# Performance work log

Hardware: AMD Instinct MI355X
Metric: run time of the kernel (lower is better)

Reference implementation:

```python
import jax, jax.numpy as jnp
import numpy as np

N_NODES = 100000
N_EDGES = 1250000
D_IN = 64
D_OUT = 64


def setup_inputs() -> dict:
    key = jax.random.key(0)
    k1, k2, k3, k4, k5 = jax.random.split(key, 5)
    x = jax.random.normal(k1, (N_NODES, D_IN), dtype=jnp.float32)
    edge_index = jax.random.randint(k2, (2, N_EDGES), 0, N_NODES, dtype=jnp.int64)
    # Linear weights stored torch-style as [out, in]
    w_neigh = jax.random.normal(k3, (D_OUT, D_IN), dtype=jnp.float32) / np.sqrt(D_IN)
    w_self = jax.random.normal(k4, (D_OUT, D_IN), dtype=jnp.float32) / np.sqrt(D_IN)
    b_self = jax.random.normal(k5, (D_OUT,), dtype=jnp.float32) * 0.01
    return {"x": x, "edge_index": edge_index, "w_neigh": w_neigh, "w_self": w_self, "b_self": b_self}


def reference(x, edge_index, w_neigh, w_self, b_self):
    num_nodes = x.shape[0]
    src, dst = edge_index[0], edge_index[1]
    # mean aggregation of neighbor features: scatter-add then divide by in-degree
    agg = jax.ops.segment_sum(x[src], dst, num_segments=num_nodes)  # [N, d]
    degree = jax.ops.segment_sum(jnp.ones_like(dst, dtype=x.dtype), dst, num_segments=num_nodes)
    degree = jnp.maximum(degree, 1.0)
    agg = agg / degree[:, None]
    return agg @ w_neigh.T + x @ w_self.T + b_self
```

## Files before the change

kernel.cpp:

```cpp
#include <hip/hip_runtime.h>

#define N_NODES 100000
#define N_EDGES 1250000
#define D 64
#define BSH 6
#define BNODES 64
#define NB 1563
#define WSW 68
#define G 512
#define CHUNK 2444
#define MM_BLOCKS ((N_NODES + 127) / 128)
#define BIN_BLOCKS 128
#define BIN_CHUNK ((N_EDGES + BIN_BLOCKS - 1) / BIN_BLOCKS)

typedef unsigned int u32;
typedef short bf16x8 __attribute__((ext_vector_type(8)));
typedef float f32x4 __attribute__((ext_vector_type(4)));

__device__ __forceinline__ u32 pack_bf16(float lo, float hi) {
    u32 a = __float_as_uint(lo);
    u32 b = __float_as_uint(hi);
    a = (a + 0x7fffu + ((a >> 16) & 1u)) >> 16;
    b = (b + 0x7fffu + ((b >> 16) & 1u)) >> 16;
    return a | (b << 16);
}

__global__ void __launch_bounds__(256) k_histw(const int* __restrict__ ei,
                                               u32* __restrict__ ghist,
                                               const float* __restrict__ wn,
                                               const float* __restrict__ wsf,
                                               u32* __restrict__ bfrag) {
    __shared__ u32 hist[NB];
    int tid = threadIdx.x;
    if (blockIdx.x < G) {
        int g = blockIdx.x;
        int e0 = g * CHUNK, e1 = min(e0 + CHUNK, N_EDGES);
        for (int i = tid; i < NB; i += 256) hist[i] = 0;
        __syncthreads();
        const int4* dp = (const int4*)(ei + N_EDGES + e0);
        int nv = (e1 - e0) >> 2;
        for (int i = tid; i < nv; i += 256) {
            int4 d4 = dp[i];
            atomicAdd(&hist[d4.x >> BSH], 1u);
            atomicAdd(&hist[d4.y >> BSH], 1u);
            atomicAdd(&hist[d4.z >> BSH], 1u);
            atomicAdd(&hist[d4.w >> BSH], 1u);
        }
        __syncthreads();
        for (int i = tid; i < NB; i += 256)
            ghist[(size_t)i * G + g] = hist[i];
    } else {
        for (int i = tid; i < 4096; i += 256) {
            int t = i >> 9, h = (i >> 8) & 1, l = (i >> 2) & 63, q = i & 3;
            int k0 = h * 32 + (l >> 4) * 8 + 2 * q;
            int n = t * 16 + (l & 15);
            const float* w = (n < 64) ? &wn[(size_t)n * 64] : &wsf[(size_t)(n - 64) * 64];
            bfrag[i] = pack_bf16(w[k0], w[k0 + 1]);
        }
    }
}

__global__ void __launch_bounds__(512) k_scanB(const u32* __restrict__ ghist,
                                               u32* __restrict__ gbase,
                                               u32* __restrict__ bcnt) {
    __shared__ u32 wt[8];
    int t = threadIdx.x;
    int b = blockIdx.x;
    int lane = t & 63, wv = t >> 6;
    u32 v = ghist[(size_t)b * G + t];
    u32 s = v;
#pragma unroll
    for (int off = 1; off < 64; off <<= 1) {
        u32 n = __shfl_up(s, off, 64);
        if (lane >= off) s += n;
    }
    if (lane == 63) wt[wv] = s;
    __syncthreads();
    u32 add = 0;
#pragma unroll
    for (int q = 0; q < 8; ++q) add += (q < wv) ? wt[q] : 0u;
    u32 incl = s + add;
    gbase[(size_t)b * G + t] = incl - v;
    if (t == G - 1) bcnt[b] = incl;
}

__global__ void __launch_bounds__(256) k_scatmm(const int* __restrict__ ei,
                                                const u32* __restrict__ gbase,
                                                u32* __restrict__ binned,
                                                int cap,
                                                const float* __restrict__ x,
                                                const u32* __restrict__ bfrag,
                                                const float* __restrict__ bias,
                                                u32* __restrict__ y16,
                                                float* __restrict__ zout) {
    __shared__ u32 cur[NB];
    int tid = threadIdx.x;
    if (blockIdx.x < G) {
        int g = blockIdx.x;
        int e0 = g * CHUNK, e1 = min(e0 + CHUNK, N_EDGES);
        for (int i = tid; i < NB; i += 256)
            cur[i] = gbase[(size_t)i * G + g];
        __syncthreads();
        const int4* sp = (const int4*)(ei + e0);
        const int4* dp = (const int4*)(ei + N_EDGES + e0);
        int nv = (e1 - e0) >> 2;
        for (int i = tid; i < nv; i += 256) {
            int4 s4 = sp[i];
            int4 d4 = dp[i];
            int ss[4] = {s4.x, s4.y, s4.z, s4.w};
            int dd[4] = {d4.x, d4.y, d4.z, d4.w};
#pragma unroll
            for (int u = 0; u < 4; ++u) {
                int b = dd[u] >> BSH;
                u32 loc = atomicAdd(&cur[b], 1u);
                if (loc < (u32)cap)
                    binned[(size_t)b * cap + loc] = ((u32)ss[u] << BSH) | (u32)(dd[u] & (BNODES - 1));
            }
        }
        return;
    }

    int w = tid >> 6, l = tid & 63;
    int lg = l >> 4, c = l & 15;
    int nodebase = (blockIdx.x - G) * 128 + w * 32;

    union FU { uint4 u; bf16x8 v; };

    bf16x8 af[2][2];
#pragma unroll
    for (int m = 0; m < 2; ++m) {
        int node = nodebase + m * 16 + c;
        if (node >= N_NODES) node = N_NODES - 1;
        const float4* xr = (const float4*)(x + (size_t)node * D);
#pragma unroll
        for (int h = 0; h < 2; ++h) {
            float4 p0 = xr[h * 8 + lg * 2];
            float4 p1 = xr[h * 8 + lg * 2 + 1];
            FU au;
            au.u.x = pack_bf16(p0.x, p0.y);
            au.u.y = pack_bf16(p0.z, p0.w);
            au.u.z = pack_bf16(p1.x, p1.y);
            au.u.w = pack_bf16(p1.z, p1.w);
            af[m][h] = au.v;
        }
    }

    f32x4 acc[2][8];
#pragma unroll
    for (int m = 0; m < 2; ++m) {
#pragma unroll
        for (int t = 0; t < 4; ++t) acc[m][t] = (f32x4){0.f, 0.f, 0.f, 0.f};
#pragma unroll
        for (int t = 4; t < 8; ++t) {
            float bb = bias[(t - 4) * 16 + c];
            acc[m][t] = (f32x4){bb, bb, bb, bb};
        }
    }

    const uint4* bp = (const uint4*)bfrag;
#pragma unroll
    for (int tc = 0; tc < 2; ++tc) {
        bf16x8 bf[4][2];
#pragma unroll
        for (int tt = 0; tt < 4; ++tt)
#pragma unroll
            for (int h = 0; h < 2; ++h) {
                FU bu;
                bu.u = bp[(((tc * 4 + tt) * 2 + h) * 64) + l];
                bf[tt][h] = bu.v;
            }
#pragma unroll
        for (int m = 0; m < 2; ++m)
#pragma unroll
            for (int tt = 0; tt < 4; ++tt) {
                int t = tc * 4 + tt;
                acc[m][t] = __builtin_amdgcn_mfma_f32_16x16x32_bf16(
                    af[m][0], bf[tt][0], acc[m][t], 0, 0, 0);
                acc[m][t] = __builtin_amdgcn_mfma_f32_16x16x32_bf16(
                    af[m][1], bf[tt][1], acc[m][t], 0, 0, 0);
            }
    }

#pragma unroll
    for (int m = 0; m < 2; ++m) {
        int rowbase = nodebase + m * 16 + lg * 4;
#pragma unroll
        for (int r = 0; r < 4; ++r) {
            int node = rowbase + r;
            bool ok = node < N_NODES;
#pragma unroll
            for (int t = 4; t < 8; ++t) {
                if (ok) zout[(size_t)node * D + (t - 4) * 16 + c] = acc[m][t][r];
            }
#pragma unroll
            for (int t = 0; t < 4; ++t) {
                float v = acc[m][t][r];
                float o = __shfl_xor(v, 1);
                if (ok && !(c & 1))
                    y16[(size_t)node * 32 + t * 8 + (c >> 1)] = pack_bf16(v, o);
            }
        }
    }
}

__global__ void __launch_bounds__(256) k_sortgather(const u32* __restrict__ y16,
                                                    const u32* __restrict__ binned,
                                                    const u32* __restrict__ bcnt,
                                                    int cap,
                                                    float* __restrict__ io) {
    __shared__ u32 eh[1024];
    __shared__ u32 srt[1024];
    __shared__ u32 hist[BNODES];
    __shared__ u32 nbase[BNODES];
    __shared__ u32 cur[BNODES];
    int tid = threadIdx.x;
    int b = blockIdx.x;
    int cnt = min((int)bcnt[b], cap);
    const u32* seg = binned + (size_t)b * cap;

    if (tid < BNODES) hist[tid] = 0;
    __syncthreads();
    const uint4* segv = (const uint4*)seg;
    int nv = cnt >> 2;
    for (int i = tid; i < nv; i += 256) {
        uint4 w4 = segv[i];
        *(uint4*)&eh[4 * i] = w4;
        atomicAdd(&hist[w4.x & (BNODES - 1)], 1u);
        atomicAdd(&hist[w4.y & (BNODES - 1)], 1u);
        atomicAdd(&hist[w4.z & (BNODES - 1)], 1u);
        atomicAdd(&hist[w4.w & (BNODES - 1)], 1u);
    }
    for (int i = (cnt & ~3) + tid; i < cnt; i += 256) {
        u32 w = seg[i];
        eh[i] = w;
        atomicAdd(&hist[w & (BNODES - 1)], 1u);
    }
    __syncthreads();
    if (tid < BNODES) {
        u32 v = hist[tid];
        u32 s = v;
#pragma unroll
        for (int off = 1; off < 64; off <<= 1) {
            u32 n = __shfl_up(s, off, 64);
            if (tid >= off) s += n;
        }
        u32 excl = s - v;
        nbase[tid] = excl;
        cur[tid] = excl;
    }
    __syncthreads();
    for (int i = tid; i < cnt; i += 256) {
        u32 w = eh[i];
        u32 p = atomicAdd(&cur[w & (BNODES - 1)], 1u);
        srt[p] = w >> BSH;
    }
    __syncthreads();

    int wv = tid >> 6, lane = tid & 63;
    int sub = lane >> 4;
    int pr = lane & 15;
    const uint2* yv = (const uint2*)y16;
    int nodebase = b << BSH;

    for (int i = 0; i < 16; ++i) {
        int dl = wv * 16 + i;
        int node = nodebase + dl;
        u32 o0 = nbase[dl];
        u32 dg = hist[dl];
        float a0 = 0.f, a1 = 0.f, a2 = 0.f, a3 = 0.f;
        for (u32 r = 0; r < dg; r += 32) {
            uint2 w[8];
#pragma unroll
            for (int t = 0; t < 8; ++t) {
                u32 e = r + 4 * t + sub;
                w[t] = make_uint2(0u, 0u);
                if (e < dg) w[t] = yv[(size_t)srt[o0 + e] * 16 + pr];
            }
#pragma unroll
            for (int t = 0; t < 8; ++t) {
                if (r + 4u * (u32)t < dg) {
                    a0 += __uint_as_float(w[t].x << 16);
                    a1 += __uint_as_float(w[t].x & 0xffff0000u);
                    a2 += __uint_as_float(w[t].y << 16);
                    a3 += __uint_as_float(w[t].y & 0xffff0000u);
                }
            }
        }
        a0 += __shfl_xor(a0, 16); a1 += __shfl_xor(a1, 16);
        a2 += __shfl_xor(a2, 16); a3 += __shfl_xor(a3, 16);
        a0 += __shfl_xor(a0, 32); a1 += __shfl_xor(a1, 32);
        a2 += __shfl_xor(a2, 32); a3 += __shfl_xor(a3, 32);
        if (sub == 0 && node < N_NODES) {
            float inv = 1.0f / (float)max(dg, 1u);
            float4 z = *(const float4*)&io[(size_t)node * D + 4 * pr];
            *(float4*)&io[(size_t)node * D + 4 * pr] =
                make_float4(z.x + a0 * inv, z.y + a1 * inv, z.z + a2 * inv, z.w + a3 * inv);
        }
    }
}

__global__ void __launch_bounds__(256) k_bin2(const int* __restrict__ ei,
                                              u32* __restrict__ bcnt,
                                              u32* __restrict__ binned,
                                              int cap) {
    __shared__ u32 hist[NB];
    __shared__ u32 rbase[NB];
    int tid = threadIdx.x;
    int e0 = blockIdx.x * BIN_CHUNK;
    int e1 = min(e0 + BIN_CHUNK, N_EDGES);
    const int* dstp = ei + N_EDGES;
    for (int i = tid; i < NB; i += 256) hist[i] = 0;
    __syncthreads();
    for (int e = e0 + tid; e < e1; e += 256)
        atomicAdd(&hist[dstp[e] >> BSH], 1u);
    __syncthreads();
    for (int i = tid; i < NB; i += 256) {
        u32 h = hist[i];
        rbase[i] = h ? atomicAdd(&bcnt[i], h) : 0u;
        hist[i] = 0;
    }
    __syncthreads();
    for (int e = e0 + tid; e < e1; e += 256) {
        int d = dstp[e];
        int s = ei[e];
        int b = d >> BSH;
        u32 loc = atomicAdd(&hist[b], 1u);
        u32 slot = rbase[b] + loc;
        if (slot < (u32)cap)
            binned[(size_t)b * cap + slot] = ((u32)s << BSH) | (u32)(d & (BNODES - 1));
    }
}

__global__ void __launch_bounds__(256) k_sort_fb(u32* __restrict__ binned,
                                                 const u32* __restrict__ bcnt,
                                                 int cap,
                                                 u32* __restrict__ offs,
                                                 u32* __restrict__ deg) {
    __shared__ u32 eh[1024];
    __shared__ u32 hist[BNODES];
    __shared__ u32 cur[BNODES];
    int tid = threadIdx.x;
    int b = blockIdx.x;
    int cnt = min((int)bcnt[b], cap);
    u32* seg = binned + (size_t)b * cap;
    if (tid < BNODES) hist[tid] = 0;
    __syncthreads();
    for (int i = tid; i < cnt; i += 256) {
        u32 w = seg[i];
        eh[i] = w;
        atomicAdd(&hist[w & (BNODES - 1)], 1u);
    }
    __syncthreads();
    if (tid < BNODES) {
        u32 v = hist[tid];
        u32 s = v;
#pragma unroll
        for (int off = 1; off < 64; off <<= 1) {
            u32 n = __shfl_up(s, off, 64);
            if (tid >= off) s += n;
        }
        u32 excl = s - v;
        cur[tid] = excl;
        int node = (b << BSH) + tid;
        if (node < N_NODES) {
            offs[node] = (u32)((size_t)b * cap + excl);
            deg[node] = v;
        }
    }
    __syncthreads();
    for (int i = tid; i < cnt; i += 256) {
        u32 w = eh[i];
        u32 p = atomicAdd(&cur[w & (BNODES - 1)], 1u);
        seg[p] = w >> BSH;
    }
}

__global__ void __launch_bounds__(256) k_gather32(const float* __restrict__ x,
                                                  const u32* __restrict__ binned,
                                                  const u32* __restrict__ offs,
                                                  const u32* __restrict__ deg,
                                                  float* __restrict__ agg) {
    int tid = blockIdx.x * 256 + threadIdx.x;
    int node = tid >> 6;
    int d = tid & 63;
    if (node >= N_NODES) return;
    u32 o0 = offs[node], dg = deg[node];
    u32 o1 = o0 + dg;
    float s = 0.f;
    u32 j = o0;
    for (; j + 8 <= o1; j += 8) {
        u32 e[8];
        float v[8];
#pragma unroll
        for (int t = 0; t < 8; ++t) e[t] = binned[j + t];
#pragma unroll
        for (int t = 0; t < 8; ++t) v[t] = x[(size_t)e[t] * D + d];
#pragma unroll
        for (int t = 0; t < 8; ++t) s += v[t];
    }
    for (; j < o1; ++j) s += x[(size_t)binned[j] * D + d];
    agg[(size_t)node * D + d] = s / (float)max(dg, 1u);
}

__global__ void __launch_bounds__(256) k_gemm_fb(const float* __restrict__ x,
                                                 const float* __restrict__ wn,
                                                 const float* __restrict__ wsf,
                                                 const float* __restrict__ bias,
                                                 float* __restrict__ io) {
    __shared__ float At[BNODES * WSW];
    __shared__ float Wt[128 * WSW];
    int tid = threadIdx.x;
    int base = blockIdx.x * 64;
    const float4* iop = (const float4*)io;
    const float4* xp  = (const float4*)x;
    for (int i = tid; i < 4096; i += 256) {
        int d = i >> 6, k = i & 63;
        Wt[k * WSW + d] = wn[i];
        Wt[(64 + k) * WSW + d] = wsf[i];
    }
    for (int i = tid; i < 1024; i += 256) {
        int r = i >> 4, q = i & 15;
        int node = base + r;
        float4 v = make_float4(0.f, 0.f, 0.f, 0.f);
        if (node < N_NODES) v = iop[(size_t)node * 16 + q];
        *(float4*)&At[r * WSW + q * 4] = v;
    }
    __syncthreads();
    int tn = tid >> 4, td = tid & 15;
    int n0 = tn * 4, d0 = td * 4;
    float4 b4 = *(const float4*)&bias[d0];
    float acc[4][4];
#pragma unroll
    for (int i = 0; i < 4; ++i) {
        acc[i][0] = b4.x; acc[i][1] = b4.y; acc[i][2] = b4.z; acc[i][3] = b4.w;
    }
#pragma unroll 8
    for (int kc = 0; kc < 16; ++kc) {
        float4 a[4], w[4];
#pragma unroll
        for (int i = 0; i < 4; ++i) a[i] = *(const float4*)&At[(n0 + i) * WSW + kc * 4];
#pragma unroll
        for (int t = 0; t < 4; ++t) w[t] = *(const float4*)&Wt[(kc * 4 + t) * WSW + d0];
#pragma unroll
        for (int i = 0; i < 4; ++i) {
            const float av[4] = {a[i].x, a[i].y, a[i].z, a[i].w};
#pragma unroll
            for (int t = 0; t < 4; ++t) {
                acc[i][0] += av[t] * w[t].x; acc[i][1] += av[t] * w[t].y;
                acc[i][2] += av[t] * w[t].z; acc[i][3] += av[t] * w[t].w;
            }
        }
    }
    __syncthreads();
    for (int i = tid; i < 1024; i += 256) {
        int r = i >> 4, q = i & 15;
        int node = base + r;
        float4 v = make_float4(0.f, 0.f, 0.f, 0.f);
        if (node < N_NODES) v = xp[(size_t)node * 16 + q];
        *(float4*)&At[r * WSW + q * 4] = v;
    }
    __syncthreads();
#pragma unroll 8
    for (int kc = 0; kc < 16; ++kc) {
        float4 a[4], w[4];
#pragma unroll
        for (int i = 0; i < 4; ++i) a[i] = *(const float4*)&At[(n0 + i) * WSW + kc * 4];
#pragma unroll
        for (int t = 0; t < 4; ++t) w[t] = *(const float4*)&Wt[(64 + kc * 4 + t) * WSW + d0];
#pragma unroll
        for (int i = 0; i < 4; ++i) {
            const float av[4] = {a[i].x, a[i].y, a[i].z, a[i].w};
#pragma unroll
            for (int t = 0; t < 4; ++t) {
                acc[i][0] += av[t] * w[t].x; acc[i][1] += av[t] * w[t].y;
                acc[i][2] += av[t] * w[t].z; acc[i][3] += av[t] * w[t].w;
            }
        }
    }
#pragma unroll
    for (int i = 0; i < 4; ++i) {
        int node = base + n0 + i;
        if (node < N_NODES) {
            *(float4*)&io[(size_t)node * D + d0] =
                make_float4(acc[i][0], acc[i][1], acc[i][2], acc[i][3]);
        }
    }
}

extern "C" void kernel_launch(void* const* d_in, const int* in_sizes, int n_in,
                              void* d_out, int out_size, void* d_ws, size_t ws_size,
                              hipStream_t stream) {
    const float* x = (const float*)d_in[0];
    const int* ei = (const int*)d_in[1];
    const float* wn = (const float*)d_in[2];
    const float* wsf = (const float*)d_in[3];
    const float* bias = (const float*)d_in[4];
    float* out = (float*)d_out;

    u32* scratch = (u32*)d_ws;
    u32* bcnt = scratch + 2 * N_NODES;
    u32* bfrag = bcnt + ((NB + 15) & ~15);
    u32* y16 = bfrag + 8192;
    const size_t Y16W = (size_t)N_NODES * (D / 2);
    u32* binned = y16 + Y16W;
    u32* ghist = binned + (size_t)NB * 1024;
    u32* gbase = ghist + (size_t)NB * G;
    size_t fixed = 2 * (size_t)N_NODES + ((NB + 15) & ~15) + 8192;
    size_t need = fixed + Y16W + (size_t)NB * 1024 + 2 * (size_t)NB * G;

    if (ws_size / 4 >= need) {
        const int cap = 1024;
        k_histw<<<G + 1, 256, 0, stream>>>(ei, ghist, wn, wsf, bfrag);
        k_scanB<<<NB, 512, 0, stream>>>(ghist, gbase, bcnt);
        k_scatmm<<<G + MM_BLOCKS, 256, 0, stream>>>(ei, gbase, binned, cap,
                                                    x, bfrag, bias, y16, out);
        k_sortgather<<<NB, 256, 0, stream>>>(y16, binned, bcnt, cap, out);
    } else {
        u32* offs = scratch;
        u32* deg = offs + N_NODES;
        binned = bfrag;
        size_t avail = ws_size / 4 - (fixed - 8192);
        size_t capz = (avail / NB) & ~(size_t)3;
        int cap = (int)(capz < 1024 ? capz : 1024);
        hipMemsetAsync(bcnt, 0, ((NB + 15) & ~15) * sizeof(u32), stream);
        k_bin2<<<BIN_BLOCKS, 256, 0, stream>>>(ei, bcnt, binned, cap);
        k_sort_fb<<<NB, 256, 0, stream>>>(binned, bcnt, cap, offs, deg);
        k_gather32<<<(N_NODES * 64) / 256, 256, 0, stream>>>(x, binned, offs, deg, out);
        k_gemm_fb<<<(N_NODES + 63) / 64, 256, 0, stream>>>(x, wn, wsf, bias, out);
    }
}
```

Measured before the change: 83.64 us.

## Replace histogram-scan-scatter pipeline with single-pass atomic bin reservation

Removes the global histogram write, the separate scan kernel and the precomputed weight fragment buffer. Each binning block builds a local histogram, reserves a contiguous range per bin with one global atomicAdd on the bin counter, then scatters edges into its reserved slots. The GEMM blocks convert weights to bf16 inline instead of reading a prepacked buffer. This cuts two kernel launches and the large ghist/gbase traffic, but adds a memset and contended global atomics, and the edge order within each bin is no longer deterministic.

```diff
diff --git a/kernel.cpp b/kernel.cpp
--- a/kernel.cpp
+++ b/kernel.cpp
@@ -7,9 +7,9 @@
 #define BNODES 64
 #define NB 1563
 #define WSW 68
-#define G 512
-#define CHUNK 2444
 #define MM_BLOCKS ((N_NODES + 127) / 128)
+#define BIN_BLOCKS2 1024
+#define BIN_CHUNK2 1224
 #define BIN_BLOCKS 128
 #define BIN_CHUNK ((N_EDGES + BIN_BLOCKS - 1) / BIN_BLOCKS)
 
@@ -25,96 +25,65 @@
     return a | (b << 16);
 }
 
-__global__ void __launch_bounds__(256) k_histw(const int* __restrict__ ei,
-                                               u32* __restrict__ ghist,
+__global__ void __launch_bounds__(256) k_binmm(const int* __restrict__ ei,
+                                               u32* __restrict__ bcnt,
+                                               u32* __restrict__ binned,
+                                               int cap,
+                                               const float* __restrict__ x,
                                                const float* __restrict__ wn,
                                                const float* __restrict__ wsf,
-                                               u32* __restrict__ bfrag) {
+                                               const float* __restrict__ bias,
+                                               u32* __restrict__ y16,
+                                               float* __restrict__ zout) {
     __shared__ u32 hist[NB];
+    __shared__ u32 rbase[NB];
     int tid = threadIdx.x;
-    if (blockIdx.x < G) {
+    if (blockIdx.x < BIN_BLOCKS2) {
         int g = blockIdx.x;
-        int e0 = g * CHUNK, e1 = min(e0 + CHUNK, N_EDGES);
+        int e0 = g * BIN_CHUNK2;
+        int e1 = min(e0 + BIN_CHUNK2, N_EDGES);
+        int ne = e1 - e0;
         for (int i = tid; i < NB; i += 256) hist[i] = 0;
         __syncthreads();
-        const int4* dp = (const int4*)(ei + N_EDGES + e0);
-        int nv = (e1 - e0) >> 2;
-        for (int i = tid; i < nv; i += 256) {
-            int4 d4 = dp[i];
-            atomicAdd(&hist[d4.x >> BSH], 1u);
-            atomicAdd(&hist[d4.y >> BSH], 1u);
-            atomicAdd(&hist[d4.z >> BSH], 1u);
-            atomicAdd(&hist[d4.w >> BSH], 1u);
+        if (ne > 0) {
+            const int4* dp = (const int4*)(ei + N_EDGES + e0);
+            int nv = ne >> 2;
+            for (int i = tid; i < nv; i += 256) {
+                int4 d4 = dp[i];
+                atomicAdd(&hist[d4.x >> BSH], 1u);
+                atomicAdd(&hist[d4.y >> BSH], 1u);
+                atomicAdd(&hist[d4.z >> BSH], 1u);
+                atomicAdd(&hist[d4.w >> BSH], 1u);
+            }
         }
         __syncthreads();
-        for (int i = tid; i < NB; i += 256)
-            ghist[(size_t)i * G + g] = hist[i];
-    } else {
-        for (int i = tid; i < 4096; i += 256) {
-            int t = i >> 9, h = (i >> 8) & 1, l = (i >> 2) & 63, q = i & 3;
-            int k0 = h * 32 + (l >> 4) * 8 + 2 * q;
-            int n = t * 16 + (l & 15);
-            const float* w = (n < 64) ? &wn[(size_t)n * 64] : &wsf[(size_t)(n - 64) * 64];
-            bfrag[i] = pack_bf16(w[k0], w[k0 + 1]);
-        }
-    }
-}
-
-__global__ void __launch_bounds__(512) k_scanB(const u32* __restrict__ ghist,
-                                               u32* __restrict__ gbase,
-                                               u32* __restrict__ bcnt) {
-    __shared__ u32 wt[8];
-    int t = threadIdx.x;
-    int b = blockIdx.x;
-    int lane = t & 63, wv = t >> 6;
-    u32 v = ghist[(size_t)b * G + t];
-    u32 s = v;
-#pragma unroll
-    for (int off = 1; off < 64; off <<= 1) {
-        u32 n = __shfl_up(s, off, 64);
-        if (lane >= off) s += n;
-    }
-    if (lane == 63) wt[wv] = s;
-    __syncthreads();
-    u32 add = 0;
-#pragma unroll
-    for (int q = 0; q < 8; ++q) add += (q < wv) ? wt[q] : 0u;
-    u32 incl = s + add;
-    gbase[(size_t)b * G + t] = incl - v;
-    if (t == G - 1) bcnt[b] = incl;
-}
-
-__global__ void __launch_bounds__(256) k_scatmm(const int* __restrict__ ei,
-                                                const u32* __restrict__ gbase,
-                                                u32* __restrict__ binned,
-                                                int cap,
-                                                const float* __restrict__ x,
-                                                const u32* __restrict__ bfrag,
-                                                const float* __restrict__ bias,
-                                                u32* __restrict__ y16,
-                                                float* __restrict__ zout) {
-    __shared__ u32 cur[NB];
-    int tid = threadIdx.x;
-    if (blockIdx.x < G) {
-        int g = blockIdx.x;
-        int e0 = g * CHUNK, e1 = min(e0 + CHUNK, N_EDGES);
-        for (int i = tid; i < NB; i += 256)
-            cur[i] = gbase[(size_t)i * G + g];
+        int rot = (g * 97) % NB;
+        for (int i = tid; i < NB; i += 256) {
+            int ii = i + rot;
+            if (ii >= NB) ii -= NB;
+            u32 h = hist[ii];
+            rbase[ii] = h ? atomicAdd(&bcnt[ii], h) : 0u;
+            hist[ii] = 0;
+        }
         __syncthreads();
-        const int4* sp = (const int4*)(ei + e0);
-        const int4* dp = (const int4*)(ei + N_EDGES + e0);
-        int nv = (e1 - e0) >> 2;
-        for (int i = tid; i < nv; i += 256) {
-            int4 s4 = sp[i];
-            int4 d4 = dp[i];
-            int ss[4] = {s4.x, s4.y, s4.z, s4.w};
-            int dd[4] = {d4.x, d4.y, d4.z, d4.w};
-#pragma unroll
-            for (int u = 0; u < 4; ++u) {
-                int b = dd[u] >> BSH;
-                u32 loc = atomicAdd(&cur[b], 1u);
-                if (loc < (u32)cap)
-                    binned[(size_t)b * cap + loc] = ((u32)ss[u] << BSH) | (u32)(dd[u] & (BNODES - 1));
+        if (ne > 0) {
+            const int4* sp = (const int4*)(ei + e0);
+            const int4* dp = (const int4*)(ei + N_EDGES + e0);
+            int nv = ne >> 2;
+            for (int i = tid; i < nv; i += 256) {
+                int4 s4 = sp[i];
+                int4 d4 = dp[i];
+                int ss[4] = {s4.x, s4.y, s4.z, s4.w};
+                int dd[4] = {d4.x, d4.y, d4.z, d4.w};
+#pragma unroll
+                for (int u = 0; u < 4; ++u) {
+                    int b = dd[u] >> BSH;
+                    u32 loc = atomicAdd(&hist[b], 1u);
+                    u32 slot = rbase[b] + loc;
+                    if (slot < (u32)cap)
+                        binned[(size_t)b * cap + slot] =
+                            ((u32)ss[u] << BSH) | (u32)(dd[u] & (BNODES - 1));
+                }
             }
         }
         return;
@@ -122,7 +91,7 @@
 
     int w = tid >> 6, l = tid & 63;
     int lg = l >> 4, c = l & 15;
-    int nodebase = (blockIdx.x - G) * 128 + w * 32;
+    int nodebase = (blockIdx.x - BIN_BLOCKS2) * 128 + w * 32;
 
     union FU { uint4 u; bf16x8 v; };
 
@@ -157,18 +126,27 @@
         }
     }
 
-    const uint4* bp = (const uint4*)bfrag;
 #pragma unroll
     for (int tc = 0; tc < 2; ++tc) {
         bf16x8 bf[4][2];
 #pragma unroll
-        for (int tt = 0; tt < 4; ++tt)
+        for (int tt = 0; tt < 4; ++tt) {
+            int n = (tc * 4 + tt) * 16 + c;
+            const float* wrow = (n < 64) ? &wn[(size_t)n * 64]
+                                         : &wsf[(size_t)(n - 64) * 64];
 #pragma unroll
             for (int h = 0; h < 2; ++h) {
+                int k0 = h * 32 + lg * 8;
+                float4 q0 = *(const float4*)&wrow[k0];
+                float4 q1 = *(const float4*)&wrow[k0 + 4];
                 FU bu;
-                bu.u = bp[(((tc * 4 + tt) * 2 + h) * 64) + l];
+                bu.u.x = pack_bf16(q0.x, q0.y);
+                bu.u.y = pack_bf16(q0.z, q0.w);
+                bu.u.z = pack_bf16(q1.x, q1.y);
+                bu.u.w = pack_bf16(q1.z, q1.w);
                 bf[tt][h] = bu.v;
             }
+        }
 #pragma unroll
         for (int m = 0; m < 2; ++m)
 #pragma unroll
@@ -499,33 +477,29 @@
 
     u32* scratch = (u32*)d_ws;
     u32* bcnt = scratch + 2 * N_NODES;
-    u32* bfrag = bcnt + ((NB + 15) & ~15);
-    u32* y16 = bfrag + 8192;
+    u32* y16 = bcnt + ((NB + 15) & ~15);
     const size_t Y16W = (size_t)N_NODES * (D / 2);
     u32* binned = y16 + Y16W;
-    u32* ghist = binned + (size_t)NB * 1024;
-    u32* gbase = ghist + (size_t)NB * G;
-    size_t fixed = 2 * (size_t)N_NODES + ((NB + 15) & ~15) + 8192;
-    size_t need = fixed + Y16W + (size_t)NB * 1024 + 2 * (size_t)NB * G;
+    size_t fixed = 2 * (size_t)N_NODES + ((NB + 15) & ~15);
+    size_t need = fixed + Y16W + (size_t)NB * 1024;
 
     if (ws_size / 4 >= need) {
         const int cap = 1024;
-        k_histw<<<G + 1, 256, 0, stream>>>(ei, ghist, wn, wsf, bfrag);
-        k_scanB<<<NB, 512, 0, stream>>>(ghist, gbase, bcnt);
-        k_scatmm<<<G + MM_BLOCKS, 256, 0, stream>>>(ei, gbase, binned, cap,
-                                                    x, bfrag, bias, y16, out);
+        hipMemsetAsync(bcnt, 0, ((NB + 15) & ~15) * sizeof(u32), stream);
+        k_binmm<<<BIN_BLOCKS2 + MM_BLOCKS, 256, 0, stream>>>(
+            ei, bcnt, binned, cap, x, wn, wsf, bias, y16, out);
         k_sortgather<<<NB, 256, 0, stream>>>(y16, binned, bcnt, cap, out);
     } else {
         u32* offs = scratch;
         u32* deg = offs + N_NODES;
-        binned = bfrag;
-        size_t avail = ws_size / 4 - (fixed - 8192);
+        u32* binned_fb = y16;
+        size_t avail = ws_size / 4 - fixed;
         size_t capz = (avail / NB) & ~(size_t)3;
         int cap = (int)(capz < 1024 ? capz : 1024);
         hipMemsetAsync(bcnt, 0, ((NB + 15) & ~15) * sizeof(u32), stream);
-        k_bin2<<<BIN_BLOCKS, 256, 0, stream>>>(ei, bcnt, binned, cap);
-        k_sort_fb<<<NB, 256, 0, stream>>>(binned, bcnt, cap, offs, deg);
-        k_gather32<<<(N_NODES * 64) / 256, 256, 0, stream>>>(x, binned, offs, deg, out);
+        k_bin2<<<BIN_BLOCKS, 256, 0, stream>>>(ei, bcnt, binned_fb, cap);
+        k_sort_fb<<<NB, 256, 0, stream>>>(binned_fb, bcnt, cap, offs, deg);
+        k_gather32<<<(N_NODES * 64) / 256, 256, 0, stream>>>(x, binned_fb, offs, deg, out);
         k_gemm_fb<<<(N_NODES + 63) / 64, 256, 0, stream>>>(x, wn, wsf, bias, out);
     }
 }
```

Result: slower. 103.6 us (+23.8%).
